# Kernel tuning notes

Measured on AMD Instinct MI355X. Metric: run time of the kernel, lower is better.

## Reference

```python
import jax, jax.numpy as jnp
import numpy as np

N_WIRES = 8
DIM = 1 << N_WIRES  # 256

# Precompute CNOT permutations (torchquantum convention: wire 0 = MSB)
_idx = np.arange(DIM)
_CNOT_PERMS = []
for _c in range(N_WIRES):
    _t = (_c + 1) % N_WIRES
    _cbit = (_idx >> (N_WIRES - 1 - _c)) & 1
    _CNOT_PERMS.append(np.where(_cbit == 1, _idx ^ (1 << (N_WIRES - 1 - _t)), _idx))
# PauliZ signs per wire: [DIM, N_WIRES]
_ZSIGNS = np.stack([1.0 - 2.0 * ((_idx >> (N_WIRES - 1 - w)) & 1) for w in range(N_WIRES)], axis=1).astype(np.float32)


def _quantum_heads(x, theta):
    """x: [B,S,H,8] angles; theta: [8]. Returns PauliZ expectations [B,S,H,8].

    Simulates per (token,head) an 8-qubit circuit: RX(x_i+theta_i) on wire i
    (encoder RX followed by trainable RX on same wire = one RX with summed angle),
    then CNOT ring 0->1..6->7, 7->0, then MeasureAll PauliZ.
    """
    B, S, H, _ = x.shape
    N = B * S * H
    ang = x.reshape(N, N_WIRES) + theta  # [N,8]
    state = jnp.zeros((N, DIM), dtype=jnp.complex64).at[:, 0].set(1.0)
    half = ang * 0.5
    c_all = jnp.cos(half)
    s_all = jnp.sin(half)
    for w in range(N_WIRES):
        A = 1 << w
        Bdim = 1 << (N_WIRES - 1 - w)
        s = state.reshape(N, A, 2, Bdim)
        a0, a1 = s[:, :, 0, :], s[:, :, 1, :]
        c = c_all[:, w][:, None, None].astype(jnp.complex64)
        isn = (1j * s_all[:, w][:, None, None]).astype(jnp.complex64)
        n0 = c * a0 - isn * a1
        n1 = -isn * a0 + c * a1
        state = jnp.stack([n0, n1], axis=2).reshape(N, DIM)
    for perm in _CNOT_PERMS:
        state = state[:, perm]
    probs = state.real ** 2 + state.imag ** 2  # [N,256]
    exp = probs @ jnp.asarray(_ZSIGNS)  # [N,8]
    return exp.reshape(B, S, H, N_WIRES)


def _mha(proj, W_combine, num_heads):
    # proj: [B,S,E]; q = k = v = proj (identical deterministic projections)
    B, S, E = proj.shape
    d_k = E // num_heads
    qkv = proj.reshape(B, S, num_heads, d_k).transpose(0, 2, 1, 3)  # [B,H,S,dk]
    scores = jnp.einsum('bhqd,bhkd->bhqk', qkv, qkv) / jnp.sqrt(jnp.float32(d_k))
    attn = jax.nn.softmax(scores, axis=-1)
    out = jnp.einsum('bhqk,bhkd->bhqd', attn, qkv)
    out = out.transpose(0, 2, 1, 3).reshape(B, S, E)
    return out @ W_combine.T


def setup_inputs() -> dict:
    key = jax.random.key(0)
    k1, k2, k3 = jax.random.split(key, 3)
    B, S, H = 8, 1024, 8
    E = H * N_WIRES  # 64
    x = jax.random.normal(k1, (B, S, E), dtype=jnp.float32)
    theta = jax.random.normal(k2, (N_WIRES,), dtype=jnp.float32)
    W_combine = jax.random.normal(k3, (E, E), dtype=jnp.float32) * (1.0 / np.sqrt(E))
    return {'x': x, 'theta': theta, 'W_combine': W_combine}


def reference(x, theta, W_combine):
    B, S, E = x.shape
    H = E // N_WIRES
    proj = _quantum_heads(x.reshape(B, S, H, N_WIRES), theta).reshape(B, S, E)
    return _mha(proj, W_combine, H)
```

## Files before the change

kernel.cpp:

```cpp
#include <hip/hip_runtime.h>

typedef _Float16 half4v __attribute__((ext_vector_type(4)));
typedef __fp16 fp16x2 __attribute__((ext_vector_type(2)));
typedef float float4v __attribute__((ext_vector_type(4)));

#define NW 8
#define S_ 1024
#define H_ 8
#define B_ 8
#define BH 64
#define NROW 8192
#define E_ 64
#define VST 1032
#define ZOFF (9 * VST)
#define NLDS (9 * VST + 16)

static __device__ inline half4v pack4(float a, float b, float c, float d) {
    union { fp16x2 f2[2]; half4v h4; } u;
    u.f2[0] = __builtin_amdgcn_cvt_pkrtz(a, b);
    u.f2[1] = __builtin_amdgcn_cvt_pkrtz(c, d);
    return u.h4;
}

__global__ __launch_bounds__(256, 4) void attn_kernel(
        const float* __restrict__ x, const float* __restrict__ theta,
        float* __restrict__ attnout) {
    __shared__ _Float16 vT[NLDS];
    int bh = blockIdx.x;
    int b = bh >> 3, h = bh & 7;
    int tid = threadIdx.x;

    float th[8];
#pragma unroll
    for (int i = 0; i < 8; ++i) th[i] = theta[i];

    {
        const half4v zer = {(_Float16)0.f, (_Float16)0.f, (_Float16)0.f, (_Float16)0.f};
        const half4v one = {(_Float16)1.f, (_Float16)1.f, (_Float16)1.f, (_Float16)1.f};
        if (tid < 4) *(half4v*)&vT[ZOFF + tid * 4] = zer;
        *(half4v*)&vT[8 * VST + tid * 4] = one;
    }

    for (int s = tid; s < S_; s += 256) {
        const float4* xp = (const float4*)(x + (((size_t)(b << 10) + s) << 6) + (h << 3));
        float4 x0 = xp[0];
        float4 x1 = xp[1];
        float c0 = __cosf(x0.x + th[0]);
        float c1 = __cosf(x0.y + th[1]);
        float c2 = __cosf(x0.z + th[2]);
        float c3 = __cosf(x0.w + th[3]);
        float c4 = __cosf(x1.x + th[4]);
        float c5 = __cosf(x1.y + th[5]);
        float c6 = __cosf(x1.z + th[6]);
        float c7 = __cosf(x1.w + th[7]);
        float e1 = c0 * c1;
        float e2 = e1 * c2;
        float e3 = e2 * c3;
        float e4 = e3 * c4;
        float e5 = e4 * c5;
        float e6 = e5 * c6;
        float e7 = e6 * c7;
        float e0 = ((c1 * c2) * (c3 * c4)) * ((c5 * c6) * c7);
        vT[0 * VST + s] = (_Float16)e0;
        vT[1 * VST + s] = (_Float16)e1;
        vT[2 * VST + s] = (_Float16)e2;
        vT[3 * VST + s] = (_Float16)e3;
        vT[4 * VST + s] = (_Float16)e4;
        vT[5 * VST + s] = (_Float16)e5;
        vT[6 * VST + s] = (_Float16)e6;
        vT[7 * VST + s] = (_Float16)e7;
    }
    __syncthreads();

    int lane = tid & 63;
    int wv   = tid >> 6;
    int col  = lane & 15;
    int quad = lane >> 4;
    int q0   = blockIdx.y * 64 + wv * 16;

    bool lo2 = (quad < 2);

    half4v qf;
    {
        int d0 = quad * 4;
        int a0 = lo2 ? ((d0 + 0) * VST + q0 + col) : (ZOFF + 0);
        int a1 = lo2 ? ((d0 + 1) * VST + q0 + col) : (ZOFF + 1);
        int a2 = lo2 ? ((d0 + 2) * VST + q0 + col) : (ZOFF + 2);
        int a3 = lo2 ? ((d0 + 3) * VST + q0 + col) : (ZOFF + 3);
        half4v t = {vT[a0], vT[a1], vT[a2], vT[a3]};
        qf = t * (_Float16)0.51012921f;
    }

    int rb0 = lo2 ? ((quad * 4 + 0) * VST) : (ZOFF + 0);
    int rb1 = lo2 ? ((quad * 4 + 1) * VST) : (ZOFF + 1);
    int rb2 = lo2 ? ((quad * 4 + 2) * VST) : (ZOFF + 2);
    int rb3 = lo2 ? ((quad * 4 + 3) * VST) : (ZOFF + 3);
    int cbase = lo2 ? col : 0;
    int cstep = lo2 ? 16 : 0;

    int vbase = (col < 9) ? (col * VST) : ZOFF;
    int vstep = (col < 9) ? 16 : 0;

#define LOADK(dst, t) { int c_ = cbase + (t) * cstep; \
        half4v r_ = {vT[rb0 + c_], vT[rb1 + c_], vT[rb2 + c_], vT[rb3 + c_]}; dst = r_; }
#define LOADV(dst, t) { dst = *(const half4v*)&vT[vbase + quad * 4 + (t) * vstep]; }

    float4v oacc = {0.f, 0.f, 0.f, 0.f};
    const float4v zc = {0.f, 0.f, 0.f, 0.f};
    const float SH = 4.08040428f;

    half4v kA, vA, kB, vB, kN, vN, kM, vM;
    LOADK(kA, 0); LOADV(vA, 0);
    LOADK(kB, 1); LOADV(vB, 1);

    for (int kt = 0; kt < 64; kt += 2) {
        float4v s0 = __builtin_amdgcn_mfma_f32_16x16x16f16(kA, qf, zc, 0, 0, 0);
        int t2 = (kt + 2) & 63;
        LOADK(kN, t2); LOADV(vN, t2);
        float p0 = __builtin_amdgcn_exp2f(s0[0] - SH);
        float p1 = __builtin_amdgcn_exp2f(s0[1] - SH);
        float p2 = __builtin_amdgcn_exp2f(s0[2] - SH);
        float p3 = __builtin_amdgcn_exp2f(s0[3] - SH);
        half4v pa = pack4(p0, p1, p2, p3);
        oacc = __builtin_amdgcn_mfma_f32_16x16x16f16(vA, pa, oacc, 0, 0, 0);
        float4v s1 = __builtin_amdgcn_mfma_f32_16x16x16f16(kB, qf, zc, 0, 0, 0);
        int t3 = (kt + 3) & 63;
        LOADK(kM, t3); LOADV(vM, t3);
        float r0 = __builtin_amdgcn_exp2f(s1[0] - SH);
        float r1 = __builtin_amdgcn_exp2f(s1[1] - SH);
        float r2 = __builtin_amdgcn_exp2f(s1[2] - SH);
        float r3 = __builtin_amdgcn_exp2f(s1[3] - SH);
        half4v pb = pack4(r0, r1, r2, r3);
        oacc = __builtin_amdgcn_mfma_f32_16x16x16f16(vB, pb, oacc, 0, 0, 0);
        kA = kN; vA = vN; kB = kM; vB = vM;
    }

    float l = __shfl(oacc[0], 32 | col, 64);
    if (lo2) {
        float inv = __builtin_amdgcn_rcpf(l);
        float4 ov = make_float4(oacc[0] * inv, oacc[1] * inv, oacc[2] * inv, oacc[3] * inv);
        *(float4*)(attnout + (((size_t)(b << 10) + q0 + col) << 6) + (h << 3) + quad * 4) = ov;
    }
#undef LOADK
#undef LOADV
}

#define CROWS 16
__global__ __launch_bounds__(256) void combine_kernel(
        const float* __restrict__ A, const float* __restrict__ W,
        float* __restrict__ out) {
    __shared__ float wl[E_ * 65];
    __shared__ float al[CROWS][E_];
    int r0 = blockIdx.x * CROWS;

    for (int idx = threadIdx.x; idx < E_ * E_; idx += 256) {
        int e = idx >> 6, k = idx & 63;
        wl[k * 65 + e] = W[idx];
    }
    ((float4*)al)[threadIdx.x] = ((const float4*)(A + (size_t)r0 * E_))[threadIdx.x];
    __syncthreads();

    int e = threadIdx.x & 63;
    int g = threadIdx.x >> 6;
    float acc[4] = {0, 0, 0, 0};
    for (int k = 0; k < E_; ++k) {
        float wv = wl[k * 65 + e];
#pragma unroll
        for (int j = 0; j < 4; ++j) acc[j] += al[g * 4 + j][k] * wv;
    }
#pragma unroll
    for (int j = 0; j < 4; ++j) {
        int r = r0 + g * 4 + j;
        out[(size_t)r * E_ + e] = acc[j];
    }
}

extern "C" void kernel_launch(void* const* d_in, const int* in_sizes, int n_in,
                              void* d_out, int out_size, void* d_ws, size_t ws_size,
                              hipStream_t stream) {
    const float* x     = (const float*)d_in[0];
    const float* theta = (const float*)d_in[1];
    const float* W     = (const float*)d_in[2];
    float* out = (float*)d_out;

    float* attnout = (float*)d_ws;

    attn_kernel<<<dim3(BH, S_ / 64), 256, 0, stream>>>(x, theta, attnout);
    combine_kernel<<<NROW / CROWS, 256, 0, stream>>>(attnout, W, out);
}
```

Measured before the change: 80.74 us.

## Double query tiles per wave, vectorize K fragments, fp16 intermediate, MFMA combine

The attention kernel now handles 32 queries per wave (128 per block), so each K/V fragment loaded from LDS feeds two score MFMAs and two PV MFMAs. This halves the number of blocks that recompute the quantum features. A second LDS copy of K in fragment-native layout turns four scalar half loads into one vector load. The attention output is stored in fp16, and the combine projection is rewritten to use 16x16x16 f16 MFMAs over 64-row tiles instead of scalar FMA. In exchange, the kernel uses more LDS and registers (launch bounds occupancy hint lowered to 2), the grid shrinks, and fp16 rounding is added to the intermediate and W.

Measured after the change: 74.20 us. -8.1%, faster.

```diff
diff --git a/kernel.cpp b/kernel.cpp
--- a/kernel.cpp
+++ b/kernel.cpp
@@ -4,16 +4,18 @@
 typedef __fp16 fp16x2 __attribute__((ext_vector_type(2)));
 typedef float float4v __attribute__((ext_vector_type(4)));
 
-#define NW 8
 #define S_ 1024
 #define H_ 8
 #define B_ 8
 #define BH 64
 #define NROW 8192
 #define E_ 64
+
 #define VST 1032
-#define ZOFF (9 * VST)
-#define NLDS (9 * VST + 16)
+#define VZOFF (9 * VST)
+#define NV (9 * VST + 16)
+#define KFZ (64 * 128)
+#define NKF (64 * 128 + 8)
 
 static __device__ inline half4v pack4(float a, float b, float c, float d) {
     union { fp16x2 f2[2]; half4v h4; } u;
@@ -22,10 +24,11 @@
     return u.h4;
 }
 
-__global__ __launch_bounds__(256, 4) void attn_kernel(
+__global__ __launch_bounds__(256, 2) void attn_kernel(
         const float* __restrict__ x, const float* __restrict__ theta,
-        float* __restrict__ attnout) {
-    __shared__ _Float16 vT[NLDS];
+        _Float16* __restrict__ attnH) {
+    __shared__ _Float16 kF[NKF];
+    __shared__ _Float16 vT[NV];
     int bh = blockIdx.x;
     int b = bh >> 3, h = bh & 7;
     int tid = threadIdx.x;
@@ -37,7 +40,8 @@
     {
         const half4v zer = {(_Float16)0.f, (_Float16)0.f, (_Float16)0.f, (_Float16)0.f};
         const half4v one = {(_Float16)1.f, (_Float16)1.f, (_Float16)1.f, (_Float16)1.f};
-        if (tid < 4) *(half4v*)&vT[ZOFF + tid * 4] = zer;
+        if (tid < 4) *(half4v*)&vT[VZOFF + tid * 4] = zer;
+        if (tid < 2) *(half4v*)&kF[KFZ + tid * 4] = zer;
         *(half4v*)&vT[8 * VST + tid * 4] = one;
     }
 
@@ -61,14 +65,15 @@
         float e6 = e5 * c6;
         float e7 = e6 * c7;
         float e0 = ((c1 * c2) * (c3 * c4)) * ((c5 * c6) * c7);
-        vT[0 * VST + s] = (_Float16)e0;
-        vT[1 * VST + s] = (_Float16)e1;
-        vT[2 * VST + s] = (_Float16)e2;
-        vT[3 * VST + s] = (_Float16)e3;
-        vT[4 * VST + s] = (_Float16)e4;
-        vT[5 * VST + s] = (_Float16)e5;
-        vT[6 * VST + s] = (_Float16)e6;
-        vT[7 * VST + s] = (_Float16)e7;
+        half4v lo = pack4(e0, e1, e2, e3);
+        half4v hi = pack4(e4, e5, e6, e7);
+        int kt = s >> 4, c = s & 15;
+        *(half4v*)&kF[kt * 128 + c * 4]      = lo;
+        *(half4v*)&kF[kt * 128 + 64 + c * 4] = hi;
+        vT[0 * VST + s] = lo[0]; vT[1 * VST + s] = lo[1];
+        vT[2 * VST + s] = lo[2]; vT[3 * VST + s] = lo[3];
+        vT[4 * VST + s] = hi[0]; vT[5 * VST + s] = hi[1];
+        vT[6 * VST + s] = hi[2]; vT[7 * VST + s] = hi[3];
     }
     __syncthreads();
 
@@ -76,36 +81,26 @@
     int wv   = tid >> 6;
     int col  = lane & 15;
     int quad = lane >> 4;
-    int q0   = blockIdx.y * 64 + wv * 16;
+    int q0   = blockIdx.y * 128 + wv * 32;
 
     bool lo2 = (quad < 2);
 
-    half4v qf;
-    {
-        int d0 = quad * 4;
-        int a0 = lo2 ? ((d0 + 0) * VST + q0 + col) : (ZOFF + 0);
-        int a1 = lo2 ? ((d0 + 1) * VST + q0 + col) : (ZOFF + 1);
-        int a2 = lo2 ? ((d0 + 2) * VST + q0 + col) : (ZOFF + 2);
-        int a3 = lo2 ? ((d0 + 3) * VST + q0 + col) : (ZOFF + 3);
-        half4v t = {vT[a0], vT[a1], vT[a2], vT[a3]};
-        qf = t * (_Float16)0.51012921f;
-    }
-
-    int rb0 = lo2 ? ((quad * 4 + 0) * VST) : (ZOFF + 0);
-    int rb1 = lo2 ? ((quad * 4 + 1) * VST) : (ZOFF + 1);
-    int rb2 = lo2 ? ((quad * 4 + 2) * VST) : (ZOFF + 2);
-    int rb3 = lo2 ? ((quad * 4 + 3) * VST) : (ZOFF + 3);
-    int cbase = lo2 ? col : 0;
-    int cstep = lo2 ? 16 : 0;
-
-    int vbase = (col < 9) ? (col * VST) : ZOFF;
+    int kfa = lo2 ? (lane * 4) : KFZ;
+    int kstep = lo2 ? 128 : 0;
+
+    half4v qfa = *(const half4v*)&kF[kfa + (q0 >> 4) * kstep];
+    half4v qfb = *(const half4v*)&kF[kfa + ((q0 >> 4) + 1) * kstep];
+    qfa *= (_Float16)0.51012921f;
+    qfb *= (_Float16)0.51012921f;
+
+    int vbase = (col < 9) ? (col * VST + quad * 4) : VZOFF;
     int vstep = (col < 9) ? 16 : 0;
 
-#define LOADK(dst, t) { int c_ = cbase + (t) * cstep; \
-        half4v r_ = {vT[rb0 + c_], vT[rb1 + c_], vT[rb2 + c_], vT[rb3 + c_]}; dst = r_; }
-#define LOADV(dst, t) { dst = *(const half4v*)&vT[vbase + quad * 4 + (t) * vstep]; }
-
-    float4v oacc = {0.f, 0.f, 0.f, 0.f};
+#define LOADK(dst, t) { dst = *(const half4v*)&kF[kfa + (t) * kstep]; }
+#define LOADV(dst, t) { dst = *(const half4v*)&vT[vbase + (t) * vstep]; }
+
+    float4v oa = {0.f, 0.f, 0.f, 0.f};
+    float4v ob = {0.f, 0.f, 0.f, 0.f};
     const float4v zc = {0.f, 0.f, 0.f, 0.f};
     const float SH = 4.08040428f;
 
@@ -114,65 +109,107 @@
     LOADK(kB, 1); LOADV(vB, 1);
 
     for (int kt = 0; kt < 64; kt += 2) {
-        float4v s0 = __builtin_amdgcn_mfma_f32_16x16x16f16(kA, qf, zc, 0, 0, 0);
+        float4v sa = __builtin_amdgcn_mfma_f32_16x16x16f16(kA, qfa, zc, 0, 0, 0);
+        float4v sb = __builtin_amdgcn_mfma_f32_16x16x16f16(kA, qfb, zc, 0, 0, 0);
         int t2 = (kt + 2) & 63;
         LOADK(kN, t2); LOADV(vN, t2);
-        float p0 = __builtin_amdgcn_exp2f(s0[0] - SH);
-        float p1 = __builtin_amdgcn_exp2f(s0[1] - SH);
-        float p2 = __builtin_amdgcn_exp2f(s0[2] - SH);
-        float p3 = __builtin_amdgcn_exp2f(s0[3] - SH);
-        half4v pa = pack4(p0, p1, p2, p3);
-        oacc = __builtin_amdgcn_mfma_f32_16x16x16f16(vA, pa, oacc, 0, 0, 0);
-        float4v s1 = __builtin_amdgcn_mfma_f32_16x16x16f16(kB, qf, zc, 0, 0, 0);
+        half4v pa = pack4(__builtin_amdgcn_exp2f(sa[0] - SH),
+                          __builtin_amdgcn_exp2f(sa[1] - SH),
+                          __builtin_amdgcn_exp2f(sa[2] - SH),
+                          __builtin_amdgcn_exp2f(sa[3] - SH));
+        half4v pb = pack4(__builtin_amdgcn_exp2f(sb[0] - SH),
+                          __builtin_amdgcn_exp2f(sb[1] - SH),
+                          __builtin_amdgcn_exp2f(sb[2] - SH),
+                          __builtin_amdgcn_exp2f(sb[3] - SH));
+        oa = __builtin_amdgcn_mfma_f32_16x16x16f16(vA, pa, oa, 0, 0, 0);
+        ob = __builtin_amdgcn_mfma_f32_16x16x16f16(vA, pb, ob, 0, 0, 0);
+        float4v sc = __builtin_amdgcn_mfma_f32_16x16x16f16(kB, qfa, zc, 0, 0, 0);
+        float4v sd = __builtin_amdgcn_mfma_f32_16x16x16f16(kB, qfb, zc, 0, 0, 0);
         int t3 = (kt + 3) & 63;
         LOADK(kM, t3); LOADV(vM, t3);
-        float r0 = __builtin_amdgcn_exp2f(s1[0] - SH);
-        float r1 = __builtin_amdgcn_exp2f(s1[1] - SH);
-        float r2 = __builtin_amdgcn_exp2f(s1[2] - SH);
-        float r3 = __builtin_amdgcn_exp2f(s1[3] - SH);
-        half4v pb = pack4(r0, r1, r2, r3);
-        oacc = __builtin_amdgcn_mfma_f32_16x16x16f16(vB, pb, oacc, 0, 0, 0);
+        half4v pc = pack4(__builtin_amdgcn_exp2f(sc[0] - SH),
+                          __builtin_amdgcn_exp2f(sc[1] - SH),
+                          __builtin_amdgcn_exp2f(sc[2] - SH),
+                          __builtin_amdgcn_exp2f(sc[3] - SH));
+        half4v pd = pack4(__builtin_amdgcn_exp2f(sd[0] - SH),
+                          __builtin_amdgcn_exp2f(sd[1] - SH),
+                          __builtin_amdgcn_exp2f(sd[2] - SH),
+                          __builtin_amdgcn_exp2f(sd[3] - SH));
+        oa = __builtin_amdgcn_mfma_f32_16x16x16f16(vB, pc, oa, 0, 0, 0);
+        ob = __builtin_amdgcn_mfma_f32_16x16x16f16(vB, pd, ob, 0, 0, 0);
         kA = kN; vA = vN; kB = kM; vB = vM;
     }
 
-    float l = __shfl(oacc[0], 32 | col, 64);
-    if (lo2) {
-        float inv = __builtin_amdgcn_rcpf(l);
-        float4 ov = make_float4(oacc[0] * inv, oacc[1] * inv, oacc[2] * inv, oacc[3] * inv);
-        *(float4*)(attnout + (((size_t)(b << 10) + q0 + col) << 6) + (h << 3) + quad * 4) = ov;
+    int lsrc = 32 | col;
+    {
+        float l = __shfl(oa[0], lsrc, 64);
+        if (lo2) {
+            float inv = __builtin_amdgcn_rcpf(l);
+            half4v ov = pack4(oa[0] * inv, oa[1] * inv, oa[2] * inv, oa[3] * inv);
+            *(half4v*)(attnH + (((size_t)(b << 10) + q0 + col) << 6) + (h << 3) + quad * 4) = ov;
+        }
+    }
+    {
+        float l = __shfl(ob[0], lsrc, 64);
+        if (lo2) {
+            float inv = __builtin_amdgcn_rcpf(l);
+            half4v ov = pack4(ob[0] * inv, ob[1] * inv, ob[2] * inv, ob[3] * inv);
+            *(half4v*)(attnH + (((size_t)(b << 10) + q0 + 16 + col) << 6) + (h << 3) + quad * 4) = ov;
+        }
     }
 #undef LOADK
 #undef LOADV
 }
 
-#define CROWS 16
 __global__ __launch_bounds__(256) void combine_kernel(
-        const float* __restrict__ A, const float* __restrict__ W,
+        const _Float16* __restrict__ AH, const float* __restrict__ W,
         float* __restrict__ out) {
-    __shared__ float wl[E_ * 65];
-    __shared__ float al[CROWS][E_];
-    int r0 = blockIdx.x * CROWS;
-
-    for (int idx = threadIdx.x; idx < E_ * E_; idx += 256) {
+    __shared__ _Float16 a2[64 * 68];
+    __shared__ _Float16 wt[64 * 68];
+    int r0 = blockIdx.x * 64;
+    int tid = threadIdx.x;
+
+    for (int idx = tid; idx < E_ * E_; idx += 256) {
         int e = idx >> 6, k = idx & 63;
-        wl[k * 65 + e] = W[idx];
-    }
-    ((float4*)al)[threadIdx.x] = ((const float4*)(A + (size_t)r0 * E_))[threadIdx.x];
+        wt[k * 68 + e] = (_Float16)W[idx];
+    }
+#pragma unroll
+    for (int j = 0; j < 4; ++j) {
+        int off = tid * 16 + j * 4;
+        int row = off >> 6, k = off & 63;
+        *(half4v*)&a2[row * 68 + k] = *(const half4v*)&AH[(size_t)r0 * E_ + off];
+    }
     __syncthreads();
 
-    int e = threadIdx.x & 63;
-    int g = threadIdx.x >> 6;
-    float acc[4] = {0, 0, 0, 0};
-    for (int k = 0; k < E_; ++k) {
-        float wv = wl[k * 65 + e];
-#pragma unroll
-        for (int j = 0; j < 4; ++j) acc[j] += al[g * 4 + j][k] * wv;
-    }
-#pragma unroll
-    for (int j = 0; j < 4; ++j) {
-        int r = r0 + g * 4 + j;
-        out[(size_t)r * E_ + e] = acc[j];
-    }
+    int lane = tid & 63;
+    int wv   = tid >> 6;
+    int col  = lane & 15;
+    int quad = lane >> 4;
+
+    half4v wf[4][4];
+#pragma unroll
+    for (int t = 0; t < 4; ++t)
+#pragma unroll
+        for (int e = 0; e < 4; ++e) {
+            int kb = (t * 16 + quad * 4) * 68 + e * 16 + col;
+            half4v w_ = {wt[kb], wt[kb + 68], wt[kb + 136], wt[kb + 204]};
+            wf[t][e] = w_;
+        }
+
+    float4v acc[4] = {{0,0,0,0},{0,0,0,0},{0,0,0,0},{0,0,0,0}};
+#pragma unroll
+    for (int t = 0; t < 4; ++t) {
+        half4v af = *(const half4v*)&a2[(wv * 16 + col) * 68 + t * 16 + quad * 4];
+#pragma unroll
+        for (int e = 0; e < 4; ++e)
+            acc[e] = __builtin_amdgcn_mfma_f32_16x16x16f16(af, wf[t][e], acc[e], 0, 0, 0);
+    }
+
+#pragma unroll
+    for (int e = 0; e < 4; ++e)
+#pragma unroll
+        for (int r = 0; r < 4; ++r)
+            out[(size_t)(r0 + wv * 16 + quad * 4 + r) * E_ + e * 16 + col] = acc[e][r];
 }
 
 extern "C" void kernel_launch(void* const* d_in, const int* in_sizes, int n_in,
@@ -183,8 +220,8 @@
     const float* W     = (const float*)d_in[2];
     float* out = (float*)d_out;
 
-    float* attnout = (float*)d_ws;
-
-    attn_kernel<<<dim3(BH, S_ / 64), 256, 0, stream>>>(x, theta, attnout);
-    combine_kernel<<<NROW / CROWS, 256, 0, stream>>>(attnout, W, out);
-}
+    _Float16* attnH = (_Float16*)d_ws;
+
+    attn_kernel<<<dim3(BH, S_ / 128), 256, 0, stream>>>(x, theta, attnH);
+    combine_kernel<<<NROW / 64, 256, 0, stream>>>(attnH, W, out);
+}
```
